# Kernel optimization log

Measured on AMD Instinct MI355X. Metric: run time of the kernel, lower is better.

The kernel has to match this reference:

```python
import jax, jax.numpy as jnp
import numpy as np

D_LATENT = 8
N_CENTERS = 48
CHANNELS = 64
PM_STEPS = 4
DT, BETA, CLAMP = 0.12, 1.0, 3.0
SIGMA_E, SIGMA_I, K_E, K_I, GAIN = 0.6, 1.2, 0.8, 1.0, 0.06


def setup_inputs() -> dict:
    key = jax.random.key(0)
    ks = jax.random.split(key, 12)
    B = 8192
    x = jax.random.normal(ks[0], (B, 784), dtype=jnp.float32)
    # encoder params (torch Linear default-ish init scale)
    W1 = jax.random.normal(ks[1], (784, 256), dtype=jnp.float32) * (1.0 / np.sqrt(784))
    b1 = jnp.zeros((256,), jnp.float32)
    W2 = jax.random.normal(ks[2], (256, D_LATENT), dtype=jnp.float32) * (1.0 / np.sqrt(256))
    b2 = jnp.zeros((D_LATENT,), jnp.float32)
    centers = jax.random.normal(ks[3], (N_CENTERS, D_LATENT), dtype=jnp.float32) * 0.7
    mus = jnp.ones((N_CENTERS,), jnp.float32) * 0.4
    projW = jax.random.normal(ks[4], (D_LATENT, CHANNELS), dtype=jnp.float32) * (1.0 / np.sqrt(D_LATENT))
    projb = jnp.zeros((CHANNELS,), jnp.float32)
    roW = jax.random.normal(ks[5], (CHANNELS, 10), dtype=jnp.float32) * (1.0 / np.sqrt(CHANNELS))
    rob = jnp.zeros((10,), jnp.float32)
    return {"x": x, "W1": W1, "b1": b1, "W2": W2, "b2": b2,
            "centers": centers, "mus": mus, "projW": projW, "projb": projb,
            "roW": roW, "rob": rob, "T": 5}


def _pm_field(z, centers, mus):
    # one PMField forward: `PM_STEPS` gradient-flow steps on z [B, d]
    for _ in range(PM_STEPS):
        diff = z[:, None, :] - centers[None, :, :]            # [B, C, d]
        r2 = jnp.sum(diff * diff, axis=-1) + 1e-4              # [B, C]
        r = jnp.sqrt(r2)
        n = 1.0 + jnp.sum(mus[None, :] / r, axis=1)            # [B]
        g = -jnp.sum(mus[None, :, None] * diff / (r * r2)[:, :, None], axis=1)  # [B, d]
        z = z + DT * BETA * (g / n[:, None])
        z = jnp.clip(z, -CLAMP, CLAMP)
    return z


def _lateral_ei(z, h):
    # kernel computed with no_grad in torch -> stop_gradient here
    sq = jnp.sum(z * z, axis=1)                                # [B]
    dist2 = jnp.maximum(sq[:, None] + sq[None, :] - 2.0 * (z @ z.T), 0.0)
    Ke = K_E * jnp.exp(-dist2 / (2.0 * SIGMA_E ** 2))
    Ki = K_I * jnp.exp(-dist2 / (2.0 * SIGMA_I ** 2))
    K = Ke - Ki
    K = K / (jnp.sum(K, axis=1, keepdims=True) + 1e-6)
    K = jax.lax.stop_gradient(K)
    return GAIN * (K @ h)


def reference(x, W1, b1, W2, b2, centers, mus, projW, projb, roW, rob, T):
    z = jnp.tanh(x @ W1 + b1) @ W2 + b2                        # encoder -> [B, d]
    h = jnp.zeros((x.shape[0], CHANNELS), x.dtype)
    logits = None
    for _ in range(T):
        z = _pm_field(z, centers, mus)
        h = 0.9 * h + 0.1 * jnp.tanh(z @ projW + projb)
        h = h + _lateral_ei(z, h)
        logits = h @ roW + rob
    return logits, z, h
```

## Files before the change

kernel.cpp:

```cpp
#include <hip/hip_runtime.h>
#include <hip/hip_bf16.h>
#include <math.h>

#define B_N      8192
#define IN_DIM   784
#define KPAD     800
#define HID      256
#define DL       8
#define NC       48
#define CH       64
#define NCLS     10
#define T_ITERS  5
#define TILES    128

#define DT_      0.12f
#define CLAMP_   3.0f
#define GAIN_    0.06f
#define SQIL2    0.70776814f
#define ONE_BF16 0x3F80u

#if defined(__has_builtin)
#if __has_builtin(__builtin_amdgcn_exp2f)
#define EXP2(x) __builtin_amdgcn_exp2f(x)
#endif
#endif
#ifndef EXP2
#define EXP2(x) exp2f(x)
#endif

typedef __attribute__((ext_vector_type(8))) short short8v;
typedef __attribute__((ext_vector_type(4))) float f32x4;

__device__ __forceinline__ unsigned int pack_bf16_rhu(float lo, float hi) {
    unsigned int b0 = __builtin_bit_cast(unsigned int, lo);
    unsigned int b1 = __builtin_bit_cast(unsigned int, hi);
    return ((b0 + 0x8000u) >> 16) | ((b1 + 0x8000u) & 0xFFFF0000u);
}
__device__ __forceinline__ unsigned short bf16_1(float x) {
    return (unsigned short)((__builtin_bit_cast(unsigned int, x) + 0x8000u) >> 16);
}
__device__ __forceinline__ float bf16_to_f(unsigned short h) {
    return __builtin_bit_cast(float, ((unsigned int)h) << 16);
}

__device__ __forceinline__ void z_split(const float4 a, const float4 b,
                                        uint4& Whi, uint4& Wlo, unsigned int& Wc)
{
    float u[8] = {SQIL2*a.x, SQIL2*a.y, SQIL2*a.z, SQIL2*a.w,
                  SQIL2*b.x, SQIL2*b.y, SQIL2*b.z, SQIL2*b.w};
    float sq = 0.f;
    #pragma unroll
    for (int d = 0; d < 8; ++d) sq = fmaf(u[d], u[d], sq);
    float cn = -0.5f * sq;
    unsigned short hi[8]; float lo[8];
    #pragma unroll
    for (int d = 0; d < 8; ++d) {
        hi[d] = bf16_1(u[d]);
        lo[d] = u[d] - bf16_to_f(hi[d]);
    }
    unsigned short ch_ = bf16_1(cn);
    unsigned short cl_ = bf16_1(cn - bf16_to_f(ch_));
    Whi.x = (unsigned int)hi[0] | ((unsigned int)hi[1] << 16);
    Whi.y = (unsigned int)hi[2] | ((unsigned int)hi[3] << 16);
    Whi.z = (unsigned int)hi[4] | ((unsigned int)hi[5] << 16);
    Whi.w = (unsigned int)hi[6] | ((unsigned int)hi[7] << 16);
    Wlo.x = pack_bf16_rhu(lo[0], lo[1]); Wlo.y = pack_bf16_rhu(lo[2], lo[3]);
    Wlo.z = pack_bf16_rhu(lo[4], lo[5]); Wlo.w = pack_bf16_rhu(lo[6], lo[7]);
    Wc = (unsigned int)ch_ | ((unsigned int)cl_ << 16);
}

__device__ __forceinline__ void split3_8(const float v[8],
                                         uint4& Th, uint4& Tm, uint4& Tl)
{
    unsigned short h8[8], m8[8], l8[8];
    #pragma unroll
    for (int d = 0; d < 8; ++d) {
        unsigned short h = bf16_1(v[d]);
        float r1 = v[d] - bf16_to_f(h);
        unsigned short m = bf16_1(r1);
        float r2 = r1 - bf16_to_f(m);
        unsigned short l = bf16_1(r2);
        h8[d] = h; m8[d] = m; l8[d] = l;
    }
    Th.x = (unsigned int)h8[0] | ((unsigned int)h8[1] << 16);
    Th.y = (unsigned int)h8[2] | ((unsigned int)h8[3] << 16);
    Th.z = (unsigned int)h8[4] | ((unsigned int)h8[5] << 16);
    Th.w = (unsigned int)h8[6] | ((unsigned int)h8[7] << 16);
    Tm.x = (unsigned int)m8[0] | ((unsigned int)m8[1] << 16);
    Tm.y = (unsigned int)m8[2] | ((unsigned int)m8[3] << 16);
    Tm.z = (unsigned int)m8[4] | ((unsigned int)m8[5] << 16);
    Tm.w = (unsigned int)m8[6] | ((unsigned int)m8[7] << 16);
    Tl.x = (unsigned int)l8[0] | ((unsigned int)l8[1] << 16);
    Tl.y = (unsigned int)l8[2] | ((unsigned int)l8[3] << 16);
    Tl.z = (unsigned int)l8[4] | ((unsigned int)l8[5] << 16);
    Tl.w = (unsigned int)l8[6] | ((unsigned int)l8[7] << 16);
}

__global__ __launch_bounds__(256) void k_w1split(
    const float* __restrict__ W1, unsigned short* __restrict__ W1aT,
    unsigned short* __restrict__ W1bT, unsigned short* __restrict__ W1cT)
{
    const int k = blockIdx.x;
    const int n = threadIdx.x;
    float v = (k < IN_DIM) ? W1[(size_t)k * HID + n] : 0.f;
    unsigned short h = bf16_1(v);
    float r1 = v - bf16_to_f(h);
    unsigned short m = bf16_1(r1);
    unsigned short l = bf16_1(r1 - bf16_to_f(m));
    W1aT[(size_t)n * KPAD + k] = h;
    W1bT[(size_t)n * KPAD + k] = m;
    W1cT[(size_t)n * KPAD + k] = l;
}

__global__ __launch_bounds__(256, 2) void k_gemm1_tanh(
    const float* __restrict__ x, const unsigned short* __restrict__ W1aT,
    const unsigned short* __restrict__ W1bT, const unsigned short* __restrict__ W1cT,
    const float* __restrict__ b1, float* __restrict__ H1)
{
    __shared__ __align__(16) unsigned short Ah[2][64][40], Am[2][64][40], Al[2][64][40];
    __shared__ __align__(16) unsigned short Bh[2][64][40], Bm[2][64][40], Bl[2][64][40];
    const int tid = threadIdx.x;
    const int row0 = blockIdx.x * 64;
    const int col0 = blockIdx.y * 64;
    const int wv = tid >> 6, lane = tid & 63;
    const int l15 = lane & 15, g = lane >> 4;
    const int sr = tid >> 2, ss = tid & 3;

    f32x4 acc[4] = {{0,0,0,0},{0,0,0,0},{0,0,0,0},{0,0,0,0}};

    {
        float xv[8];
        {
            const float* xp = x + (size_t)(row0 + sr) * IN_DIM + ss * 8;
            float4 a = *(const float4*)(xp), b = *(const float4*)(xp + 4);
            xv[0]=a.x; xv[1]=a.y; xv[2]=a.z; xv[3]=a.w;
            xv[4]=b.x; xv[5]=b.y; xv[6]=b.z; xv[7]=b.w;
        }
        uint4 Th, Tm, Tl;
        split3_8(xv, Th, Tm, Tl);
        *(uint4*)&Ah[0][sr][ss * 8] = Th;
        *(uint4*)&Am[0][sr][ss * 8] = Tm;
        *(uint4*)&Al[0][sr][ss * 8] = Tl;
        const size_t wo = (size_t)(col0 + sr) * KPAD + ss * 8;
        *(uint4*)&Bh[0][sr][ss * 8] = *(const uint4*)(W1aT + wo);
        *(uint4*)&Bm[0][sr][ss * 8] = *(const uint4*)(W1bT + wo);
        *(uint4*)&Bl[0][sr][ss * 8] = *(const uint4*)(W1cT + wo);
    }

    const int NK = KPAD / 32;
    #pragma unroll 1
    for (int ks = 0; ks < NK; ++ks) {
        const int cur = ks & 1;
        const bool more = (ks + 1 < NK);
        float xv[8];
        uint4 wa4, wb4, wc4;
        if (more) {
            const int k0 = (ks + 1) * 32;
            if (k0 + ss * 8 < IN_DIM) {
                const float* xp = x + (size_t)(row0 + sr) * IN_DIM + k0 + ss * 8;
                float4 a = *(const float4*)(xp), b = *(const float4*)(xp + 4);
                xv[0]=a.x; xv[1]=a.y; xv[2]=a.z; xv[3]=a.w;
                xv[4]=b.x; xv[5]=b.y; xv[6]=b.z; xv[7]=b.w;
            } else {
                #pragma unroll
                for (int d = 0; d < 8; ++d) xv[d] = 0.f;
            }
            const size_t wo = (size_t)(col0 + sr) * KPAD + k0 + ss * 8;
            wa4 = *(const uint4*)(W1aT + wo);
            wb4 = *(const uint4*)(W1bT + wo);
            wc4 = *(const uint4*)(W1cT + wo);
        }
        __syncthreads();

        short8v ah = *(const short8v*)&Ah[cur][16 * wv + l15][g * 8];
        short8v am = *(const short8v*)&Am[cur][16 * wv + l15][g * 8];
        short8v al = *(const short8v*)&Al[cur][16 * wv + l15][g * 8];
        __builtin_amdgcn_s_setprio(1);
        #pragma unroll
        for (int nt = 0; nt < 4; ++nt) {
            short8v bh = *(const short8v*)&Bh[cur][nt * 16 + l15][g * 8];
            short8v bm = *(const short8v*)&Bm[cur][nt * 16 + l15][g * 8];
            short8v bl = *(const short8v*)&Bl[cur][nt * 16 + l15][g * 8];
            acc[nt] = __builtin_amdgcn_mfma_f32_16x16x32_bf16(ah, bh, acc[nt], 0, 0, 0);
            acc[nt] = __builtin_amdgcn_mfma_f32_16x16x32_bf16(am, bh, acc[nt], 0, 0, 0);
            acc[nt] = __builtin_amdgcn_mfma_f32_16x16x32_bf16(ah, bm, acc[nt], 0, 0, 0);
            acc[nt] = __builtin_amdgcn_mfma_f32_16x16x32_bf16(al, bh, acc[nt], 0, 0, 0);
            acc[nt] = __builtin_amdgcn_mfma_f32_16x16x32_bf16(am, bm, acc[nt], 0, 0, 0);
            acc[nt] = __builtin_amdgcn_mfma_f32_16x16x32_bf16(ah, bl, acc[nt], 0, 0, 0);
        }
        __builtin_amdgcn_s_setprio(0);

        if (more) {
            const int nb = cur ^ 1;
            uint4 Th, Tm, Tl;
            split3_8(xv, Th, Tm, Tl);
            *(uint4*)&Ah[nb][sr][ss * 8] = Th;
            *(uint4*)&Am[nb][sr][ss * 8] = Tm;
            *(uint4*)&Al[nb][sr][ss * 8] = Tl;
            *(uint4*)&Bh[nb][sr][ss * 8] = wa4;
            *(uint4*)&Bm[nb][sr][ss * 8] = wb4;
            *(uint4*)&Bl[nb][sr][ss * 8] = wc4;
        }
    }

    #pragma unroll
    for (int nt = 0; nt < 4; ++nt) {
        const int cc = col0 + nt * 16 + l15;
        const float bc = b1[cc];
        #pragma unroll
        for (int r = 0; r < 4; ++r) {
            const int rr = row0 + 16 * wv + g * 4 + r;
            H1[(size_t)rr * HID + cc] = tanhf(acc[nt][r] + bc);
        }
    }
}

__global__ __launch_bounds__(256) void k_gemm2(
    const float* __restrict__ H1, const float* __restrict__ W2,
    const float* __restrict__ b2, float* __restrict__ zbuf)
{
    __shared__ float W2s[HID][DL];
    const int tid = threadIdx.x;
    for (int l = tid; l < HID * DL; l += 256) W2s[l >> 3][l & 7] = W2[l];
    __syncthreads();
    const int row = blockIdx.x * 32 + (tid >> 3);
    const int d = tid & 7;
    float acc = b2[d];
    const float* hr = H1 + (size_t)row * HID;
    for (int k = 0; k < HID; k += 4) {
        float4 hv = *(const float4*)(hr + k);
        acc += hv.x * W2s[k][d] + hv.y * W2s[k+1][d]
             + hv.z * W2s[k+2][d] + hv.w * W2s[k+3][d];
    }
    zbuf[(size_t)row * DL + d] = acc;
}

template<int S, bool HP>
__global__ __launch_bounds__(256) void k_pm_proj(
    const float* __restrict__ centers, const float* __restrict__ mus,
    const float* __restrict__ projW, const float* __restrict__ projb,
    float* __restrict__ zbuf, float* __restrict__ hB,
    unsigned short* __restrict__ hTb, unsigned short* __restrict__ zAg,
    const float* __restrict__ pAcc, const float* __restrict__ pDen)
{
    __shared__ float4 cs4[NC][2];
    __shared__ float mu_s[NC];
    __shared__ float pW[DL][CH];
    __shared__ float pb[CH];
    const int tid = threadIdx.x;
    for (int l = tid; l < NC * 2; l += 256) cs4[l >> 1][l & 1] = ((const float4*)centers)[l];
    if (tid < NC) mu_s[tid] = mus[tid];
    for (int l = tid; l < DL * CH; l += 256) pW[l >> 6][l & 63] = projW[l];
    if (tid < CH) pb[tid] = projb[tid];
    __syncthreads();

    const int rloc = tid >> 4;
    const int ln   = tid & 15;
    const int row  = blockIdx.x * 16 + rloc;

    float4 cza[3], czb[3];
    float mur[3];
    #pragma unroll
    for (int k = 0; k < 3; ++k) {
        cza[k] = cs4[ln + 16*k][0];
        czb[k] = cs4[ln + 16*k][1];
        mur[k] = mu_s[ln + 16*k];
    }

    float z[8];
    {
        const float4* zp = (const float4*)(zbuf + (size_t)row * DL);
        float4 a = zp[0], b = zp[1];
        z[0]=a.x; z[1]=a.y; z[2]=a.z; z[3]=a.w;
        z[4]=b.x; z[5]=b.y; z[6]=b.z; z[7]=b.w;
    }

    #pragma unroll
    for (int step = 0; step < 4; ++step) {
        float np = 0.f;
        float gp[8] = {0,0,0,0,0,0,0,0};
        #pragma unroll
        for (int k = 0; k < 3; ++k) {
            float d0 = z[0]-cza[k].x, d1 = z[1]-cza[k].y;
            float d2 = z[2]-cza[k].z, d3 = z[3]-cza[k].w;
            float d4 = z[4]-czb[k].x, d5 = z[5]-czb[k].y;
            float d6 = z[6]-czb[k].z, d7 = z[7]-czb[k].w;
            float r2 = 1e-4f;
            r2 = fmaf(d0,d0,r2); r2 = fmaf(d1,d1,r2);
            r2 = fmaf(d2,d2,r2); r2 = fmaf(d3,d3,r2);
            r2 = fmaf(d4,d4,r2); r2 = fmaf(d5,d5,r2);
            r2 = fmaf(d6,d6,r2); r2 = fmaf(d7,d7,r2);
            float r = sqrtf(r2);
            float mr = mur[k] / r;
            np += mr;
            float t = mr / r2;
            gp[0] = fmaf(-t, d0, gp[0]); gp[1] = fmaf(-t, d1, gp[1]);
            gp[2] = fmaf(-t, d2, gp[2]); gp[3] = fmaf(-t, d3, gp[3]);
            gp[4] = fmaf(-t, d4, gp[4]); gp[5] = fmaf(-t, d5, gp[5]);
            gp[6] = fmaf(-t, d6, gp[6]); gp[7] = fmaf(-t, d7, gp[7]);
        }
        #pragma unroll
        for (int m = 1; m < 16; m <<= 1) {
            np += __shfl_xor(np, m);
            #pragma unroll
            for (int d = 0; d < 8; ++d) gp[d] += __shfl_xor(gp[d], m);
        }
        float s = DT_ / (1.f + np);
        #pragma unroll
        for (int d = 0; d < 8; ++d) {
            z[d] = fmaf(s, gp[d], z[d]);
            z[d] = fminf(fmaxf(z[d], -CLAMP_), CLAMP_);
        }
    }

    if (ln < 8) {
        float zout = z[0];
        #pragma unroll
        for (int d = 1; d < 8; ++d) zout = (ln == d) ? z[d] : zout;
        zbuf[(size_t)row * DL + ln] = zout;
    }

    if (ln < 3) {
        float4 a4 = {z[0], z[1], z[2], z[3]};
        float4 b4 = {z[4], z[5], z[6], z[7]};
        uint4 Whi, Wlo; unsigned int Wc;
        z_split(a4, b4, Whi, Wlo, Wc);
        uint4 Wa; Wa.x = Wc; Wa.y = ONE_BF16 | (ONE_BF16 << 16); Wa.z = 0; Wa.w = 0;
        uint4 outv = (ln == 0) ? Whi : ((ln == 1) ? Wlo : Wa);
        *(uint4*)(zAg + (size_t)row * 24 + ln * 8) = outv;
    }

    const int c0 = ln * 4;
    float hin[4];
    if (HP) {
        float den = 1e-6f;
        #pragma unroll
        for (int s = 0; s < S; ++s) den += pDen[s * B_N + row];
        float inv = GAIN_ / den;
        float4 a = {0.f, 0.f, 0.f, 0.f};
        #pragma unroll
        for (int s = 0; s < S; ++s) {
            float4 p = *(const float4*)(pAcc + (size_t)s * B_N * CH
                                        + (size_t)row * CH + c0);
            a.x += p.x; a.y += p.y; a.z += p.z; a.w += p.w;
        }
        float4 hm = *(const float4*)(hB + (size_t)row * CH + c0);
        hin[0] = fmaf(inv, a.x, hm.x);
        hin[1] = fmaf(inv, a.y, hm.y);
        hin[2] = fmaf(inv, a.z, hm.z);
        hin[3] = fmaf(inv, a.w, hm.w);
    } else {
        #pragma unroll
        for (int k = 0; k < 4; ++k) hin[k] = 0.f;
    }
    #pragma unroll
    for (int k = 0; k < 4; ++k) {
        int c = c0 + k;
        float s = pb[c];
        #pragma unroll
        for (int dd = 0; dd < DL; ++dd) s = fmaf(z[dd], pW[dd][c], s);
        hin[k] = 0.9f * hin[k] + 0.1f * tanhf(s);
    }
    float4 o0 = {hin[0], hin[1], hin[2], hin[3]};
    *(float4*)(hB + (size_t)row * CH + c0) = o0;

    {
        const int jl = row & 63;
        const int colp = (jl & 35) | ((jl & 12) << 1) | ((jl & 16) >> 2);
        const size_t tb = (size_t)(row & ~63) + colp;
        #pragma unroll
        for (int k = 0; k < 4; ++k)
            hTb[(size_t)(c0 + k) * B_N + tb] = bf16_1(hin[k]);
    }
}

template<int S>
__global__ __launch_bounds__(256, 4) void k_lateral(
    const unsigned short* __restrict__ zAg, const unsigned short* __restrict__ hTb,
    float* __restrict__ pAcc, float* __restrict__ pDen)
{
    __shared__ __align__(16) unsigned short hsT[2][CH][72];
    const int tid  = threadIdx.x;
    const int lane = tid & 63;
    const int wv   = tid >> 6;
    const int l15  = lane & 15;
    const int g    = lane >> 4;
    const int rowbase = blockIdx.x * 64;
    const int t0 = (TILES * blockIdx.y) / S;
    const int t1 = (TILES * (blockIdx.y + 1)) / S;
    const int chS = tid >> 2, segS = tid & 3;

    union u4s8 { uint4 u; short8v v; };

    short8v bZ;
    {
        const int bsel = (g == 2) ? 1 : ((g == 3) ? 2 : 0);
        u4s8 b4;
        b4.u = *(const uint4*)(zAg + (size_t)(rowbase + 16 * wv + l15) * 24 + bsel * 8);
        if (g == 3) { unsigned int t_ = b4.u.x; b4.u.x = b4.u.y; b4.u.y = t_; }
        bZ = b4.v;
    }
    const int asel = (g == 1) ? 1 : ((g == 3) ? 2 : 0);

    short8v bones;
    {
        u4s8 uo;
        uo.u.x = uo.u.y = uo.u.z = uo.u.w = ONE_BF16 | (ONE_BF16 << 16);
        bones = uo.v;
    }

    f32x4 acc0 = {0,0,0,0}, acc1 = {0,0,0,0}, acc2 = {0,0,0,0}, acc3 = {0,0,0,0};
    f32x4 acc4 = {0,0,0,0};
    const f32x4 zc = {0,0,0,0};

    uint4 az4[4];
    {
        const int jb = t0 * 64;
        #pragma unroll
        for (int t = 0; t < 4; ++t)
            az4[t] = *(const uint4*)(zAg + (size_t)(jb + t * 16 + l15) * 24 + asel * 8);
        const unsigned short* hs = hTb + (size_t)chS * B_N + jb + segS * 16;
        *(uint4*)(&hsT[0][chS][segS * 16])     = *(const uint4*)(hs);
        *(uint4*)(&hsT[0][chS][segS * 16 + 8]) = *(const uint4*)(hs + 8);
    }

    #pragma unroll 1
    for (int jt = t0; jt < t1; ++jt) {
        const int cur = (jt - t0) & 1;
        const bool more = (jt + 1 < t1);
        uint4 h0n, h1n, azn0, azn1, azn2, azn3;
        if (more) {
            const int jb2 = (jt + 1) * 64;
            const unsigned short* hs = hTb + (size_t)chS * B_N + jb2 + segS * 16;
            h0n = *(const uint4*)(hs);
            h1n = *(const uint4*)(hs + 8);
            azn0 = *(const uint4*)(zAg + (size_t)(jb2 +  0 + l15) * 24 + asel * 8);
            azn1 = *(const uint4*)(zAg + (size_t)(jb2 + 16 + l15) * 24 + asel * 8);
            azn2 = *(const uint4*)(zAg + (size_t)(jb2 + 32 + l15) * 24 + asel * 8);
            azn3 = *(const uint4*)(zAg + (size_t)(jb2 + 48 + l15) * 24 + asel * 8);
        }
        __syncthreads();

        f32x4 gac[4];
        __builtin_amdgcn_s_setprio(1);
        #pragma unroll
        for (int t = 0; t < 4; ++t) {
            u4s8 az; az.u = az4[t];
            gac[t] = __builtin_amdgcn_mfma_f32_16x16x32_bf16(az.v, bZ, zc, 0, 0, 0);
        }
        __builtin_amdgcn_s_setprio(0);

        short8v afr[2];
        #pragma unroll
        for (int kb = 0; kb < 2; ++kb) {
            float w8[8];
            #pragma unroll
            for (int m = 0; m < 8; ++m) {
                float out = gac[2 * kb + (m >> 2)][m & 3];
                float e1 = EXP2(out);
                float e2 = e1 * e1;
                float e4 = e2 * e2;
                float e8 = e4 * e4;
                w8[m] = fmaf(0.8f, e8, -e2);
            }
            u4s8 uf;
            uf.u.x = pack_bf16_rhu(w8[0], w8[1]);
            uf.u.y = pack_bf16_rhu(w8[2], w8[3]);
            uf.u.z = pack_bf16_rhu(w8[4], w8[5]);
            uf.u.w = pack_bf16_rhu(w8[6], w8[7]);
            afr[kb] = uf.v;
        }

        __builtin_amdgcn_s_setprio(1);
        #pragma unroll
        for (int kb = 0; kb < 2; ++kb) {
            const int jo = kb * 32 + g * 8;
            short8v b0 = *(const short8v*)&hsT[cur][ 0 + l15][jo];
            short8v b1 = *(const short8v*)&hsT[cur][16 + l15][jo];
            short8v b2 = *(const short8v*)&hsT[cur][32 + l15][jo];
            short8v b3 = *(const short8v*)&hsT[cur][48 + l15][jo];
            acc0 = __builtin_amdgcn_mfma_f32_16x16x32_bf16(afr[kb], b0, acc0, 0, 0, 0);
            acc1 = __builtin_amdgcn_mfma_f32_16x16x32_bf16(afr[kb], b1, acc1, 0, 0, 0);
            acc2 = __builtin_amdgcn_mfma_f32_16x16x32_bf16(afr[kb], b2, acc2, 0, 0, 0);
            acc3 = __builtin_amdgcn_mfma_f32_16x16x32_bf16(afr[kb], b3, acc3, 0, 0, 0);
            acc4 = __builtin_amdgcn_mfma_f32_16x16x32_bf16(afr[kb], bones, acc4, 0, 0, 0);
        }
        __builtin_amdgcn_s_setprio(0);

        if (more) {
            const int nb = cur ^ 1;
            *(uint4*)(&hsT[nb][chS][segS * 16])     = h0n;
            *(uint4*)(&hsT[nb][chS][segS * 16 + 8]) = h1n;
            az4[0] = azn0; az4[1] = azn1; az4[2] = azn2; az4[3] = azn3;
        }
    }

    float* pA = pAcc + (size_t)blockIdx.y * (B_N * CH) + (size_t)rowbase * CH;
    #pragma unroll
    for (int r = 0; r < 4; ++r) {
        int gi = 16 * wv + g * 4 + r;
        pA[(size_t)gi * CH +  0 + l15] = acc0[r];
        pA[(size_t)gi * CH + 16 + l15] = acc1[r];
        pA[(size_t)gi * CH + 32 + l15] = acc2[r];
        pA[(size_t)gi * CH + 48 + l15] = acc3[r];
    }
    if (l15 == 0) {
        #pragma unroll
        for (int r = 0; r < 4; ++r)
            pDen[blockIdx.y * B_N + rowbase + 16 * wv + g * 4 + r] = acc4[r];
    }
}

template<int S>
__global__ __launch_bounds__(256) void k_logits_h(
    const float* __restrict__ hmid, const float* __restrict__ pAcc,
    const float* __restrict__ pDen, const float* __restrict__ roW,
    const float* __restrict__ rob, float* __restrict__ out_logits,
    float* __restrict__ out_h)
{
    __shared__ float hsh[64][68];
    __shared__ float ro[CH][NCLS];
    __shared__ float rb[NCLS];
    const int tid = threadIdx.x;
    for (int l = tid; l < CH * NCLS; l += 256) ro[l / NCLS][l % NCLS] = roW[l];
    if (tid < NCLS) rb[tid] = rob[tid];
    const int rowbase = blockIdx.x * 64;
    const int r  = tid >> 2;
    const int c0 = (tid & 3) * 16;
    const int row = rowbase + r;
    float den = 1e-6f;
    #pragma unroll
    for (int s = 0; s < S; ++s) den += pDen[s * B_N + row];
    float inv = GAIN_ / den;
    #pragma unroll
    for (int q = 0; q < 4; ++q) {
        float4 a = {0.f, 0.f, 0.f, 0.f};
        #pragma unroll
        for (int s = 0; s < S; ++s) {
            float4 p = *(const float4*)(pAcc + (size_t)s * B_N * CH
                                        + (size_t)row * CH + c0 + q * 4);
            a.x += p.x; a.y += p.y; a.z += p.z; a.w += p.w;
        }
        float4 hm = *(const float4*)(hmid + (size_t)row * CH + c0 + q * 4);
        float4 hv;
        hv.x = fmaf(inv, a.x, hm.x); hv.y = fmaf(inv, a.y, hm.y);
        hv.z = fmaf(inv, a.z, hm.z); hv.w = fmaf(inv, a.w, hm.w);
        *(float4*)(&hsh[r][c0 + q * 4]) = hv;
        *(float4*)(out_h + (size_t)row * CH + c0 + q * 4) = hv;
    }
    __syncthreads();
    for (int idx = tid; idx < 64 * NCLS; idx += 256) {
        int rr = idx / NCLS, o = idx % NCLS;
        float s = rb[o];
        #pragma unroll
        for (int k = 0; k < CH; ++k) s = fmaf(hsh[rr][k], ro[k][o], s);
        out_logits[(size_t)(rowbase + rr) * NCLS + o] = s;
    }
}

template<int S>
static void run_all(const float* x, const float* W1, const float* b1,
                    const float* W2, const float* b2, const float* centers,
                    const float* mus, const float* projW, const float* projb,
                    const float* roW, const float* rob,
                    float* ws, float* out, hipStream_t stream)
{
    float* pAcc = ws;
    float* pDen = ws + (size_t)S * B_N * CH;
    float* zbuf = pDen + (size_t)S * B_N;
    float* hB   = zbuf + B_N * DL;
    unsigned short* hTb  = (unsigned short*)(hB + B_N * CH);
    unsigned short* zAg  = hTb + (size_t)B_N * CH;
    unsigned short* W1aT = zAg + (size_t)B_N * 24;
    unsigned short* W1bT = W1aT + (size_t)HID * KPAD;
    unsigned short* W1cT = W1bT + (size_t)HID * KPAD;
    float* H1   = ws;

    float* out_logits = out;
    float* out_z      = out + 81920;
    float* out_h      = out_z + 65536;

    k_w1split<<<KPAD, HID, 0, stream>>>(W1, W1aT, W1bT, W1cT);
    k_gemm1_tanh<<<dim3(B_N / 64, HID / 64), 256, 0, stream>>>(x, W1aT, W1bT, W1cT, b1, H1);
    k_gemm2<<<B_N / 32, 256, 0, stream>>>(H1, W2, b2, zbuf);

    for (int t = 0; t < T_ITERS; ++t) {
        if (t == 0)
            k_pm_proj<S, false><<<B_N / 16, 256, 0, stream>>>(
                centers, mus, projW, projb, zbuf, hB, hTb, zAg, pAcc, pDen);
        else
            k_pm_proj<S, true><<<B_N / 16, 256, 0, stream>>>(
                centers, mus, projW, projb, zbuf, hB, hTb, zAg, pAcc, pDen);
        k_lateral<S><<<dim3(TILES, S), 256, 0, stream>>>(zAg, hTb, pAcc, pDen);
    }

    k_logits_h<S><<<TILES, 256, 0, stream>>>(hB, pAcc, pDen, roW, rob,
                                             out_logits, out_h);
    hipMemcpyAsync(out_z, zbuf, (size_t)B_N * DL * sizeof(float),
                   hipMemcpyDeviceToDevice, stream);
}

extern "C" void kernel_launch(void* const* d_in, const int* in_sizes, int n_in,
                              void* d_out, int out_size, void* d_ws, size_t ws_size,
                              hipStream_t stream)
{
    const float* x       = (const float*)d_in[0];
    const float* W1      = (const float*)d_in[1];
    const float* b1      = (const float*)d_in[2];
    const float* W2      = (const float*)d_in[3];
    const float* b2      = (const float*)d_in[4];
    const float* centers = (const float*)d_in[5];
    const float* mus     = (const float*)d_in[6];
    const float* projW   = (const float*)d_in[7];
    const float* projb   = (const float*)d_in[8];
    const float* roW     = (const float*)d_in[9];
    const float* rob     = (const float*)d_in[10];

    float* ws  = (float*)d_ws;
    float* out = (float*)d_out;

    const size_t extraW = (size_t)B_N * 12 + (size_t)3 * HID * KPAD / 2;
    const size_t needS8 = ((size_t)8*B_N*CH + 8*B_N + B_N*DL + B_N*CH + B_N*CH/2 + extraW) * 4;
    const size_t needS4 = ((size_t)4*B_N*CH + 4*B_N + B_N*DL + B_N*CH + B_N*CH/2 + extraW) * 4;

    if (ws_size >= needS8)
        run_all<8>(x, W1, b1, W2, b2, centers, mus, projW, projb, roW, rob, ws, out, stream);
    else if (ws_size >= needS4)
        run_all<4>(x, W1, b1, W2, b2, centers, mus, projW, projb, roW, rob, ws, out, stream);
    else
        run_all<2>(x, W1, b1, W2, b2, centers, mus, projW, projb, roW, rob, ws, out, stream);
}
```

Before: 267.8 us.

## Fuse gemm2, PM/lateral iterations and logits into one cooperative kernel

Replaces the sequence of about a dozen small kernel launches (gemm2, five pm_proj/lateral pairs, logits) with a single persistent cooperative kernel that uses grid-wide syncs between phases. The goal is to remove per-launch overhead and inter-kernel gaps. H1 moves to its own workspace region so it no longer aliases pAcc. The fallback path keeps the old multi-launch schedule when cooperative launch is unavailable. In exchange, the fused kernel is capped at 4 blocks per CU and pays for grid.sync barriers.

```diff
diff --git a/kernel.cpp b/kernel.cpp
--- a/kernel.cpp
+++ b/kernel.cpp
@@ -1,6 +1,9 @@
 #include <hip/hip_runtime.h>
 #include <hip/hip_bf16.h>
+#include <hip/hip_cooperative_groups.h>
 #include <math.h>
+
+namespace cg = cooperative_groups;
 
 #define B_N      8192
 #define IN_DIM   784
@@ -235,28 +238,17 @@
     zbuf[(size_t)row * DL + d] = acc;
 }
 
-template<int S, bool HP>
-__global__ __launch_bounds__(256) void k_pm_proj(
-    const float* __restrict__ centers, const float* __restrict__ mus,
-    const float* __restrict__ projW, const float* __restrict__ projb,
-    float* __restrict__ zbuf, float* __restrict__ hB,
-    unsigned short* __restrict__ hTb, unsigned short* __restrict__ zAg,
-    const float* __restrict__ pAcc, const float* __restrict__ pDen)
-{
-    __shared__ float4 cs4[NC][2];
-    __shared__ float mu_s[NC];
-    __shared__ float pW[DL][CH];
-    __shared__ float pb[CH];
-    const int tid = threadIdx.x;
-    for (int l = tid; l < NC * 2; l += 256) cs4[l >> 1][l & 1] = ((const float4*)centers)[l];
-    if (tid < NC) mu_s[tid] = mus[tid];
-    for (int l = tid; l < DL * CH; l += 256) pW[l >> 6][l & 63] = projW[l];
-    if (tid < CH) pb[tid] = projb[tid];
-    __syncthreads();
-
+template<int S>
+__device__ __forceinline__ void pm_body(
+    int bid, int tid, bool hp,
+    const float4 (*cs4)[2], const float* mu_s,
+    const float (*pW)[CH], const float* pb,
+    float* zbuf, float* hB, unsigned short* hTb,
+    unsigned short* zAg, const float* pAcc, const float* pDen)
+{
     const int rloc = tid >> 4;
     const int ln   = tid & 15;
-    const int row  = blockIdx.x * 16 + rloc;
+    const int row  = bid * 16 + rloc;
 
     float4 cza[3], czb[3];
     float mur[3];
@@ -293,11 +285,11 @@
             float r = sqrtf(r2);
             float mr = mur[k] / r;
             np += mr;
-            float t = mr / r2;
-            gp[0] = fmaf(-t, d0, gp[0]); gp[1] = fmaf(-t, d1, gp[1]);
-            gp[2] = fmaf(-t, d2, gp[2]); gp[3] = fmaf(-t, d3, gp[3]);
-            gp[4] = fmaf(-t, d4, gp[4]); gp[5] = fmaf(-t, d5, gp[5]);
-            gp[6] = fmaf(-t, d6, gp[6]); gp[7] = fmaf(-t, d7, gp[7]);
+            float tt = mr / r2;
+            gp[0] = fmaf(-tt, d0, gp[0]); gp[1] = fmaf(-tt, d1, gp[1]);
+            gp[2] = fmaf(-tt, d2, gp[2]); gp[3] = fmaf(-tt, d3, gp[3]);
+            gp[4] = fmaf(-tt, d4, gp[4]); gp[5] = fmaf(-tt, d5, gp[5]);
+            gp[6] = fmaf(-tt, d6, gp[6]); gp[7] = fmaf(-tt, d7, gp[7]);
         }
         #pragma unroll
         for (int m = 1; m < 16; m <<= 1) {
@@ -332,7 +324,7 @@
 
     const int c0 = ln * 4;
     float hin[4];
-    if (HP) {
+    if (hp) {
         float den = 1e-6f;
         #pragma unroll
         for (int s = 0; s < S; ++s) den += pDen[s * B_N + row];
@@ -375,19 +367,18 @@
 }
 
 template<int S>
-__global__ __launch_bounds__(256, 4) void k_lateral(
-    const unsigned short* __restrict__ zAg, const unsigned short* __restrict__ hTb,
-    float* __restrict__ pAcc, float* __restrict__ pDen)
-{
-    __shared__ __align__(16) unsigned short hsT[2][CH][72];
-    const int tid  = threadIdx.x;
+__device__ __forceinline__ void lat_body(
+    int ib, int sp, int tid, unsigned short (*hsT)[CH][72],
+    const unsigned short* zAg, const unsigned short* hTb,
+    float* pAcc, float* pDen)
+{
     const int lane = tid & 63;
     const int wv   = tid >> 6;
     const int l15  = lane & 15;
     const int g    = lane >> 4;
-    const int rowbase = blockIdx.x * 64;
-    const int t0 = (TILES * blockIdx.y) / S;
-    const int t1 = (TILES * (blockIdx.y + 1)) / S;
+    const int rowbase = ib * 64;
+    const int t0 = (TILES * sp) / S;
+    const int t1 = (TILES * (sp + 1)) / S;
     const int chS = tid >> 2, segS = tid & 3;
 
     union u4s8 { uint4 u; short8v v; };
@@ -417,8 +408,8 @@
     {
         const int jb = t0 * 64;
         #pragma unroll
-        for (int t = 0; t < 4; ++t)
-            az4[t] = *(const uint4*)(zAg + (size_t)(jb + t * 16 + l15) * 24 + asel * 8);
+        for (int tt = 0; tt < 4; ++tt)
+            az4[tt] = *(const uint4*)(zAg + (size_t)(jb + tt * 16 + l15) * 24 + asel * 8);
         const unsigned short* hs = hTb + (size_t)chS * B_N + jb + segS * 16;
         *(uint4*)(&hsT[0][chS][segS * 16])     = *(const uint4*)(hs);
         *(uint4*)(&hsT[0][chS][segS * 16 + 8]) = *(const uint4*)(hs + 8);
@@ -444,9 +435,9 @@
         f32x4 gac[4];
         __builtin_amdgcn_s_setprio(1);
         #pragma unroll
-        for (int t = 0; t < 4; ++t) {
-            u4s8 az; az.u = az4[t];
-            gac[t] = __builtin_amdgcn_mfma_f32_16x16x32_bf16(az.v, bZ, zc, 0, 0, 0);
+        for (int tt = 0; tt < 4; ++tt) {
+            u4s8 az; az.u = az4[tt];
+            gac[tt] = __builtin_amdgcn_mfma_f32_16x16x32_bf16(az.v, bZ, zc, 0, 0, 0);
         }
         __builtin_amdgcn_s_setprio(0);
 
@@ -495,7 +486,7 @@
         }
     }
 
-    float* pA = pAcc + (size_t)blockIdx.y * (B_N * CH) + (size_t)rowbase * CH;
+    float* pA = pAcc + (size_t)sp * (B_N * CH) + (size_t)rowbase * CH;
     #pragma unroll
     for (int r = 0; r < 4; ++r) {
         int gi = 16 * wv + g * 4 + r;
@@ -507,8 +498,38 @@
     if (l15 == 0) {
         #pragma unroll
         for (int r = 0; r < 4; ++r)
-            pDen[blockIdx.y * B_N + rowbase + 16 * wv + g * 4 + r] = acc4[r];
-    }
+            pDen[sp * B_N + rowbase + 16 * wv + g * 4 + r] = acc4[r];
+    }
+}
+
+template<int S, bool HP>
+__global__ __launch_bounds__(256) void k_pm_proj(
+    const float* __restrict__ centers, const float* __restrict__ mus,
+    const float* __restrict__ projW, const float* __restrict__ projb,
+    float* __restrict__ zbuf, float* __restrict__ hB,
+    unsigned short* __restrict__ hTb, unsigned short* __restrict__ zAg,
+    const float* __restrict__ pAcc, const float* __restrict__ pDen)
+{
+    __shared__ float4 cs4[NC][2];
+    __shared__ float mu_s[NC];
+    __shared__ float pW[DL][CH];
+    __shared__ float pb[CH];
+    const int tid = threadIdx.x;
+    for (int l = tid; l < NC * 2; l += 256) cs4[l >> 1][l & 1] = ((const float4*)centers)[l];
+    if (tid < NC) mu_s[tid] = mus[tid];
+    for (int l = tid; l < DL * CH; l += 256) pW[l >> 6][l & 63] = projW[l];
+    if (tid < CH) pb[tid] = projb[tid];
+    __syncthreads();
+    pm_body<S>(blockIdx.x, tid, HP, cs4, mu_s, pW, pb, zbuf, hB, hTb, zAg, pAcc, pDen);
+}
+
+template<int S>
+__global__ __launch_bounds__(256, 4) void k_lateral(
+    const unsigned short* __restrict__ zAg, const unsigned short* __restrict__ hTb,
+    float* __restrict__ pAcc, float* __restrict__ pDen)
+{
+    __shared__ __align__(16) unsigned short hsT[2][CH][72];
+    lat_body<S>(blockIdx.x, blockIdx.y, threadIdx.x, hsT, zAg, hTb, pAcc, pDen);
 }
 
 template<int S>
@@ -559,6 +580,99 @@
 }
 
 template<int S>
+__global__ __launch_bounds__(256, 4) void k_fused(
+    const float* H1, const float* W2, const float* b2,
+    const float* centers, const float* mus,
+    const float* projW, const float* projb,
+    const float* roW, const float* rob,
+    float* zbuf, float* hB,
+    unsigned short* hTb, unsigned short* zAg,
+    float* pAcc, float* pDen,
+    float* out_logits, float* out_h)
+{
+    cg::grid_group grid = cg::this_grid();
+    const int bid = blockIdx.x;
+    const int tid = threadIdx.x;
+
+    __shared__ float4 cs4[NC][2];
+    __shared__ float mu_s[NC];
+    __shared__ float pW[DL][CH];
+    __shared__ float pb[CH];
+    __shared__ union __align__(16) {
+        unsigned short hsT[2][CH][72];
+        struct { float hsh[64][68]; float ro[CH][NCLS]; float rb[NCLS]; } lg;
+        float W2s[HID][DL];
+    } su;
+
+    for (int l = tid; l < NC * 2; l += 256) cs4[l >> 1][l & 1] = ((const float4*)centers)[l];
+    if (tid < NC) mu_s[tid] = mus[tid];
+    for (int l = tid; l < DL * CH; l += 256) pW[l >> 6][l & 63] = projW[l];
+    if (tid < CH) pb[tid] = projb[tid];
+
+    if (bid < 256) {
+        for (int l = tid; l < HID * DL; l += 256) su.W2s[l >> 3][l & 7] = W2[l];
+        __syncthreads();
+        const int row = bid * 32 + (tid >> 3);
+        const int d = tid & 7;
+        float acc = b2[d];
+        const float* hr = H1 + (size_t)row * HID;
+        for (int k = 0; k < HID; k += 4) {
+            float4 hv = *(const float4*)(hr + k);
+            acc += hv.x * su.W2s[k][d] + hv.y * su.W2s[k+1][d]
+                 + hv.z * su.W2s[k+2][d] + hv.w * su.W2s[k+3][d];
+        }
+        zbuf[(size_t)row * DL + d] = acc;
+    }
+    grid.sync();
+
+    #pragma unroll 1
+    for (int t = 0; t < T_ITERS; ++t) {
+        if (bid < 512)
+            pm_body<S>(bid, tid, t > 0, cs4, mu_s, pW, pb, zbuf, hB, hTb, zAg, pAcc, pDen);
+        grid.sync();
+        lat_body<S>(bid & (TILES - 1), bid >> 7, tid, su.hsT, zAg, hTb, pAcc, pDen);
+        grid.sync();
+    }
+
+    if (bid < 128) {
+        const int rowbase = bid * 64;
+        for (int l = tid; l < CH * NCLS; l += 256) su.lg.ro[l / NCLS][l % NCLS] = roW[l];
+        if (tid < NCLS) su.lg.rb[tid] = rob[tid];
+        const int r  = tid >> 2;
+        const int c0 = (tid & 3) * 16;
+        const int row = rowbase + r;
+        float den = 1e-6f;
+        #pragma unroll
+        for (int s = 0; s < S; ++s) den += pDen[s * B_N + row];
+        float inv = GAIN_ / den;
+        #pragma unroll
+        for (int q = 0; q < 4; ++q) {
+            float4 a = {0.f, 0.f, 0.f, 0.f};
+            #pragma unroll
+            for (int s = 0; s < S; ++s) {
+                float4 p = *(const float4*)(pAcc + (size_t)s * B_N * CH
+                                            + (size_t)row * CH + c0 + q * 4);
+                a.x += p.x; a.y += p.y; a.z += p.z; a.w += p.w;
+            }
+            float4 hm = *(const float4*)(hB + (size_t)row * CH + c0 + q * 4);
+            float4 hv;
+            hv.x = fmaf(inv, a.x, hm.x); hv.y = fmaf(inv, a.y, hm.y);
+            hv.z = fmaf(inv, a.z, hm.z); hv.w = fmaf(inv, a.w, hm.w);
+            *(float4*)(&su.lg.hsh[r][c0 + q * 4]) = hv;
+            *(float4*)(out_h + (size_t)row * CH + c0 + q * 4) = hv;
+        }
+        __syncthreads();
+        for (int idx = tid; idx < 64 * NCLS; idx += 256) {
+            int rr = idx / NCLS, o = idx % NCLS;
+            float s = su.lg.rb[o];
+            #pragma unroll
+            for (int k = 0; k < CH; ++k) s = fmaf(su.lg.hsh[rr][k], su.lg.ro[k][o], s);
+            out_logits[(size_t)(rowbase + rr) * NCLS + o] = s;
+        }
+    }
+}
+
+template<int S>
 static void run_all(const float* x, const float* W1, const float* b1,
                     const float* W2, const float* b2, const float* centers,
                     const float* mus, const float* projW, const float* projb,
@@ -574,7 +688,7 @@
     unsigned short* W1aT = zAg + (size_t)B_N * 24;
     unsigned short* W1bT = W1aT + (size_t)HID * KPAD;
     unsigned short* W1cT = W1bT + (size_t)HID * KPAD;
-    float* H1   = ws;
+    float* H1 = (float*)(W1cT + (size_t)HID * KPAD);
 
     float* out_logits = out;
     float* out_z      = out + 81920;
@@ -582,20 +696,48 @@
 
     k_w1split<<<KPAD, HID, 0, stream>>>(W1, W1aT, W1bT, W1cT);
     k_gemm1_tanh<<<dim3(B_N / 64, HID / 64), 256, 0, stream>>>(x, W1aT, W1bT, W1cT, b1, H1);
-    k_gemm2<<<B_N / 32, 256, 0, stream>>>(H1, W2, b2, zbuf);
-
-    for (int t = 0; t < T_ITERS; ++t) {
-        if (t == 0)
-            k_pm_proj<S, false><<<B_N / 16, 256, 0, stream>>>(
-                centers, mus, projW, projb, zbuf, hB, hTb, zAg, pAcc, pDen);
-        else
-            k_pm_proj<S, true><<<B_N / 16, 256, 0, stream>>>(
-                centers, mus, projW, projb, zbuf, hB, hTb, zAg, pAcc, pDen);
-        k_lateral<S><<<dim3(TILES, S), 256, 0, stream>>>(zAg, hTb, pAcc, pDen);
-    }
-
-    k_logits_h<S><<<TILES, 256, 0, stream>>>(hB, pAcc, pDen, roW, rob,
-                                             out_logits, out_h);
+
+    bool coop = false;
+    {
+        int dev = 0;
+        if (hipGetDevice(&dev) == hipSuccess) {
+            int attr = 0, ncu = 0, nb = 0;
+            hipDeviceGetAttribute(&attr, hipDeviceAttributeCooperativeLaunch, dev);
+            hipDeviceGetAttribute(&ncu, hipDeviceAttributeMultiprocessorCount, dev);
+            hipError_t q = hipOccupancyMaxActiveBlocksPerMultiprocessor(
+                &nb, k_fused<S>, 256, 0);
+            coop = (attr != 0) && (q == hipSuccess) && ((size_t)nb * ncu >= TILES * S);
+        }
+    }
+
+    if (coop) {
+        const float* H1c = H1;
+        void* kargs[] = {
+            (void*)&H1c, (void*)&W2, (void*)&b2, (void*)&centers, (void*)&mus,
+            (void*)&projW, (void*)&projb, (void*)&roW, (void*)&rob,
+            (void*)&zbuf, (void*)&hB, (void*)&hTb, (void*)&zAg,
+            (void*)&pAcc, (void*)&pDen, (void*)&out_logits, (void*)&out_h };
+        hipError_t lerr = hipLaunchCooperativeKernel(
+            reinterpret_cast<void*>(&k_fused<S>), dim3(TILES * S), dim3(256),
+            kargs, 0, stream);
+        if (lerr != hipSuccess) coop = false;
+    }
+
+    if (!coop) {
+        k_gemm2<<<B_N / 32, 256, 0, stream>>>(H1, W2, b2, zbuf);
+        for (int t = 0; t < T_ITERS; ++t) {
+            if (t == 0)
+                k_pm_proj<S, false><<<B_N / 16, 256, 0, stream>>>(
+                    centers, mus, projW, projb, zbuf, hB, hTb, zAg, pAcc, pDen);
+            else
+                k_pm_proj<S, true><<<B_N / 16, 256, 0, stream>>>(
+                    centers, mus, projW, projb, zbuf, hB, hTb, zAg, pAcc, pDen);
+            k_lateral<S><<<dim3(TILES, S), 256, 0, stream>>>(zAg, hTb, pAcc, pDen);
+        }
+        k_logits_h<S><<<TILES, 256, 0, stream>>>(hB, pAcc, pDen, roW, rob,
+                                                 out_logits, out_h);
+    }
+
     hipMemcpyAsync(out_z, zbuf, (size_t)B_N * DL * sizeof(float),
                    hipMemcpyDeviceToDevice, stream);
 }
@@ -619,7 +761,7 @@
     float* ws  = (float*)d_ws;
     float* out = (float*)d_out;
 
-    const size_t extraW = (size_t)B_N * 12 + (size_t)3 * HID * KPAD / 2;
+    const size_t extraW = (size_t)B_N * 12 + (size_t)3 * HID * KPAD / 2 + (size_t)B_N * HID;
     const size_t needS8 = ((size_t)8*B_N*CH + 8*B_N + B_N*DL + B_N*CH + B_N*CH/2 + extraW) * 4;
     const size_t needS4 = ((size_t)4*B_N*CH + 4*B_N + B_N*DL + B_N*CH + B_N*CH/2 + extraW) * 4;
 
```

Result: no change. 267.3 us (-0.2%).
